# Performance work log

Measured on AMD Instinct MI355X. Metric: run time of the kernel, lower is better.

The kernel has to match this reference:

```python
import jax, jax.numpy as jnp
import numpy as np

B, L, H, M, V = 8, 1024, 1024, 128, 32
LN_EPS = 1e-5


def setup_inputs() -> dict:
    key = jax.random.key(0)
    ks = jax.random.split(key, 6)
    x_enc = jax.random.normal(ks[0], (B, L, H), dtype=jnp.float32)
    ln_gamma = jnp.ones((H,), jnp.float32)
    ln_beta = jnp.zeros((H,), jnp.float32)
    Wq = jax.random.normal(ks[1], (H, H), jnp.float32) * 0.02
    Wk = jax.random.normal(ks[2], (H, H), jnp.float32) * 0.02
    W_embed = jax.random.normal(ks[3], (V * V, H), jnp.float32) * 0.02
    W_mlm = jax.random.normal(ks[4], (V, H), jnp.float32) * 0.02
    # masked positions per sequence: contiguous span [1, M] (token 0 at pos 0,
    # token 2 at pos M+1 in the original encoding); sorted, in-range, static M.
    mask_idx = jnp.tile(jnp.arange(1, M + 1, dtype=jnp.int32)[None, :], (B, 1))
    return {"x_enc": x_enc, "ln_gamma": ln_gamma, "ln_beta": ln_beta,
            "Wq": Wq, "Wk": Wk, "W_embed": W_embed, "W_mlm": W_mlm,
            "mask_idx": mask_idx}


def _layer_norm(x, gamma, beta):
    mu = jnp.mean(x, axis=-1, keepdims=True)
    var = jnp.mean(jnp.square(x - mu), axis=-1, keepdims=True)
    return (x - mu) * jax.lax.rsqrt(var + LN_EPS) * gamma + beta


def reference(x_enc, ln_gamma, ln_beta, Wq, Wk, W_embed, W_mlm, mask_idx):
    x = _layer_norm(x_enc, ln_gamma, ln_beta)            # [B,L,H]
    mlm_logits = jnp.einsum('blh,vh->blv', x, W_mlm)      # [B,L,V]

    # ragged masked-span gather (static M masked positions per sequence)
    masked_x = jnp.take_along_axis(x, mask_idx[:, :, None].astype(jnp.int32), axis=1)  # [B,M,H]
    q = jnp.einsum('bmh,oh->bmo', masked_x, Wq)           # fc_pmlm_q, no bias
    k = jnp.einsum('bmh,oh->bmo', masked_x, Wk)           # fc_pmlm_k, no bias
    pairs = jnp.einsum('bih,bjh->bijh', q, k)             # per-span outer product [B,M,M,H]
    pairs = pairs.reshape(B * M * M, H)
    logits = jnp.einsum('nh,vh->nv', pairs, W_embed)      # [B*M*M, V*V]

    diag_mask = jnp.tile(jnp.eye(M, dtype=bool).reshape(-1), B)  # [B*M*M]

    in_span = jnp.zeros((B, L), jnp.int8).at[jnp.arange(B)[:, None], mask_idx].set(1)
    mask_aa = in_span[:, :, None]                                      # [B,L,1]
    pair_mask_aa = (in_span[:, :, None] * in_span[:, None, :])[..., None]  # [B,L,L,1] int8

    return logits, mlm_logits, diag_mask, mask_aa, pair_mask_aa
```

## Files before the change

kernel.cpp:

```cpp
#include <hip/hip_runtime.h>


typedef float   f32x4 __attribute__((ext_vector_type(4)));
typedef _Float16 f16x8 __attribute__((ext_vector_type(8)));

__device__ __forceinline__ void gld16(const void* g, void* l) {
  __builtin_amdgcn_global_load_lds(
      (const __attribute__((address_space(1))) void*)g,
      (__attribute__((address_space(3))) void*)l, 16, 0, 0);
}

__global__ __launch_bounds__(256) void cvt_kernel(
    const float* __restrict__ wq, const float* __restrict__ wk,
    const float* __restrict__ we, const float* __restrict__ wm,
    _Float16* __restrict__ oq, _Float16* __restrict__ ok,
    _Float16* __restrict__ oe, _Float16* __restrict__ om) {
  int id = blockIdx.x * 256 + threadIdx.x;
  const float* src; _Float16* dst; int off;
  if (id < 262144)      { src = wq; dst = oq; off = id; }
  else if (id < 524288) { src = wk; dst = ok; off = id - 262144; }
  else if (id < 786432) { src = we; dst = oe; off = id - 524288; }
  else                  { src = wm; dst = om; off = id - 786432; }
  float4 v = ((const float4*)src)[off];
  union { _Float16 h[4]; uint2 u; } o;
  o.h[0] = (_Float16)v.x; o.h[1] = (_Float16)v.y;
  o.h[2] = (_Float16)v.z; o.h[3] = (_Float16)v.w;
  ((uint2*)dst)[off] = o.u;
}

__global__ __launch_bounds__(256) void ln_kernel(
    const float* __restrict__ x, const float* __restrict__ g,
    const float* __restrict__ be, _Float16* __restrict__ xo) {
  const int row = blockIdx.x, t = threadIdx.x;
  const float4 v = ((const float4*)(x + (size_t)row * 1024))[t];
  float s1 = v.x + v.y + v.z + v.w;
  float s2 = v.x * v.x + v.y * v.y + v.z * v.z + v.w * v.w;
  #pragma unroll
  for (int m = 1; m < 64; m <<= 1) {
    s1 += __shfl_xor(s1, m, 64);
    s2 += __shfl_xor(s2, m, 64);
  }
  __shared__ float red[8];
  const int w = t >> 6, lane = t & 63;
  if (lane == 0) { red[w * 2] = s1; red[w * 2 + 1] = s2; }
  __syncthreads();
  s1 = red[0] + red[2] + red[4] + red[6];
  s2 = red[1] + red[3] + red[5] + red[7];
  const float mu = s1 * (1.f / 1024.f);
  const float var = s2 * (1.f / 1024.f) - mu * mu;
  const float rs = rsqrtf(var + 1e-5f);
  const float4 gv = ((const float4*)g)[t];
  const float4 bv = ((const float4*)be)[t];
  union { _Float16 h[4]; uint2 u; } o;
  o.h[0] = (_Float16)((v.x - mu) * rs * gv.x + bv.x);
  o.h[1] = (_Float16)((v.y - mu) * rs * gv.y + bv.y);
  o.h[2] = (_Float16)((v.z - mu) * rs * gv.z + bv.z);
  o.h[3] = (_Float16)((v.w - mu) * rs * gv.w + bv.w);
  ((uint2*)(xo + (size_t)row * 1024))[t] = o.u;
}

__global__ __launch_bounds__(256, 4) void qk_gemm(
    const _Float16* __restrict__ xh, const _Float16* __restrict__ wq,
    const _Float16* __restrict__ wk, const int* __restrict__ midx,
    _Float16* __restrict__ qout, _Float16* __restrict__ kout) {
  __shared__ _Float16 at[64 * 32];
  __shared__ _Float16 bt[64 * 32];
  const int tid = threadIdx.x, w = tid >> 6, lane = tid & 63;
  const int l15 = lane & 15, quad = lane >> 4;
  const int ntile = blockIdx.x, rtile = blockIdx.y, mat = blockIdx.z;
  const _Float16* wmat = mat ? wk : wq;
  _Float16* outp = mat ? kout : qout;

  const int arow = tid >> 2;
  const int acol = (tid & 3) * 8;
  const int grow = rtile * 64 + arow;
  const int b = grow >> 7, m = grow & 127;
  const int src = midx[b * 128 + m];
  const _Float16* agp = xh + ((size_t)(b * 1024 + src)) * 1024 + acol;
  const _Float16* bgp = wmat + (size_t)(ntile * 64 + arow) * 1024 + acol;
  char* aldst = (char*)at + w * 1024;
  char* bldst = (char*)bt + w * 1024;

  f32x4 acc[4];
  const f32x4 zero = {0.f, 0.f, 0.f, 0.f};
  #pragma unroll
  for (int ns = 0; ns < 4; ++ns) acc[ns] = zero;

  for (int s = 0; s < 32; ++s) {
    const int kk = s * 32;
    gld16(agp + kk, aldst);
    gld16(bgp + kk, bldst);
    __syncthreads();
    const f16x8 af = *(const f16x8*)&at[(w * 16 + l15) * 32 + quad * 8];
    #pragma unroll
    for (int ns = 0; ns < 4; ++ns) {
      const f16x8 bf = *(const f16x8*)&bt[(ns * 16 + l15) * 32 + quad * 8];
      acc[ns] = __builtin_amdgcn_mfma_f32_16x16x32_f16(af, bf, acc[ns], 0, 0, 0);
    }
    __syncthreads();
  }
  #pragma unroll
  for (int ns = 0; ns < 4; ++ns) {
    const int col = ntile * 64 + ns * 16 + l15;
    #pragma unroll
    for (int r = 0; r < 4; ++r) {
      const int row = rtile * 64 + w * 16 + quad * 4 + r;
      outp[(size_t)row * 1024 + col] = (_Float16)acc[ns][r];
    }
  }
}

#define BG_BUF 49152
#define BG_Q   147456
#define BG_WE  16384
__global__ __launch_bounds__(512, 2) void big_gemm(
    const _Float16* __restrict__ qf, const _Float16* __restrict__ kf,
    const _Float16* __restrict__ wemb, float* __restrict__ out) {
  __shared__ __align__(16) char lds[155648];
  const int tid = threadIdx.x;
  const int w = tid >> 6, lane = tid & 63;
  const int l15 = lane & 15, quad = lane >> 4;
  const int wm = w >> 2, wn = w & 3;
  const int bid = blockIdx.x;
  const int vtile = bid & 3;
  const int grp = bid >> 2;
  const int b = grp >> 3;
  const int i0base = (grp & 7) * 16;

  const int lrow = lane >> 3;
  const int cgsw = (lane & 7) ^ lrow;
  const char* kg = (const char*)(kf + (size_t)b * 128 * 1024);
  const char* wg = (const char*)(wemb + (size_t)vtile * 256 * 1024);
  const char* ks0 = kg + (size_t)(((w)      * 8 + lrow) * 2048 + cgsw * 16);
  const char* ks1 = kg + (size_t)(((w + 8)  * 8 + lrow) * 2048 + cgsw * 16);
  const char* ws0 = wg + (size_t)(((w)      * 8 + lrow) * 2048 + cgsw * 16);
  const char* ws1 = wg + (size_t)(((w + 8)  * 8 + lrow) * 2048 + cgsw * 16);
  const char* ws2 = wg + (size_t)(((w + 16) * 8 + lrow) * 2048 + cgsw * 16);
  const char* ws3 = wg + (size_t)(((w + 24) * 8 + lrow) * 2048 + cgsw * 16);
  const int kd0 = w * 1024,          kd1 = (w + 8) * 1024;
  const int wd0 = BG_WE + w * 1024,  wd1 = BG_WE + (w + 8) * 1024;
  const int wd2 = BG_WE + (w + 16) * 1024, wd3 = BG_WE + (w + 24) * 1024;

  const char* qsp = (const char*)(qf + (size_t)(b * 128 + i0base) * 1024)
                    + (w >> 1) * 2048 + (w & 1) * 1024 + lane * 16;

  const int swzb = (l15 & 7) << 4;
  const int col0 = (quad * 16) ^ swzb;
  const int col1 = (64 + quad * 16) ^ swzb;
  const int abase = l15 * 128;
  const int bbase = BG_WE + (wn * 64 + l15) * 128;
  const int qrd = BG_Q + wm * 2048 + quad * 16;

  if (w < 4) gld16(qsp, lds + BG_Q + w * 1024);
  gld16(ks0, lds + kd0);              gld16(ks1, lds + kd1);
  gld16(ws0, lds + wd0);              gld16(ws1, lds + wd1);
  gld16(ws2, lds + wd2);              gld16(ws3, lds + wd3);
  gld16(ks0 + 128, lds + BG_BUF + kd0); gld16(ks1 + 128, lds + BG_BUF + kd1);
  gld16(ws0 + 128, lds + BG_BUF + wd0); gld16(ws1 + 128, lds + BG_BUF + wd1);
  gld16(ws2 + 128, lds + BG_BUF + wd2); gld16(ws3 + 128, lds + BG_BUF + wd3);

  f32x4 acc[8][4];
  #pragma unroll
  for (int a = 0; a < 8; ++a)
    #pragma unroll
    for (int c = 0; c < 4; ++c) acc[a][c] = (f32x4){0.f, 0.f, 0.f, 0.f};

  f16x8 af[4][2], bf0[2][2], bf1[2][2], qs0, qs1;

#define RD_A(mh)                                                               \
  _Pragma("unroll")                                                            \
  for (int ms = 0; ms < 4; ++ms) {                                             \
    af[ms][0] = *(const f16x8*)(lds + cb + abase + (mh) * 8192 + ms * 2048 + col0); \
    af[ms][1] = *(const f16x8*)(lds + cb + abase + (mh) * 8192 + ms * 2048 + col1); \
  }
#define RD_B(dst, nh)                                                          \
  _Pragma("unroll")                                                            \
  for (int ns = 0; ns < 2; ++ns) {                                             \
    dst[ns][0] = *(const f16x8*)(lds + cb + bbase + (nh) * 4096 + ns * 2048 + col0); \
    dst[ns][1] = *(const f16x8*)(lds + cb + bbase + (nh) * 4096 + ns * 2048 + col1); \
  }
#define MULT_A()                                                               \
  _Pragma("unroll")                                                            \
  for (int ms = 0; ms < 4; ++ms) { af[ms][0] *= qs0; af[ms][1] *= qs1; }
#define MFMA8(MH, NH, BFR)                                                     \
  _Pragma("unroll")                                                            \
  for (int kh = 0; kh < 2; ++kh)                                               \
    _Pragma("unroll")                                                          \
    for (int ms = 0; ms < 4; ++ms)                                             \
      _Pragma("unroll")                                                        \
      for (int ns = 0; ns < 2; ++ns)                                           \
        acc[(MH) * 4 + ms][(NH) * 2 + ns] = __builtin_amdgcn_mfma_f32_16x16x32_f16( \
            af[ms][kh], BFR[ns][kh], acc[(MH) * 4 + ms][(NH) * 2 + ns], 0, 0, 0);
#define BAR() __builtin_amdgcn_s_barrier()
#define LGKM0() asm volatile("s_waitcnt lgkmcnt(0)" ::: "memory")

  int cur = 0;
  #pragma unroll 1
  for (int T = 0; T < 128; ++T) {
    const int cb = cur * BG_BUF;
    int stg = cur + 2; if (stg >= 3) stg -= 3;
    const int sb = stg * BG_BUF;
    const int j = T >> 4, tt = T & 15;
    const int skb = ((T + 2) & 15) * 128;
    const bool st = (T < 126);
    const bool stq = (w < 4) && (((T + 2) & 15) == 0) && (T + 2 < 128);

    if (T < 127) asm volatile("s_waitcnt vmcnt(6)" ::: "memory");
    else         asm volatile("s_waitcnt vmcnt(0)" ::: "memory");
    BAR();

    qs0 = *(const f16x8*)(lds + qrd + (j & 1) * 4096 + tt * 128);
    qs1 = *(const f16x8*)(lds + qrd + (j & 1) * 4096 + tt * 128 + 64);
    RD_A(0)
    RD_B(bf0, 0)
    if (stq) gld16(qsp + (T + 2) * 256,
                   lds + BG_Q + ((((T + 2) >> 4) & 1) * 4096) + w * 1024);
    if (st) { gld16(ks0 + skb, lds + sb + kd0); gld16(ks1 + skb, lds + sb + kd1); }
    BAR(); LGKM0();
    __builtin_amdgcn_s_setprio(1);
    MULT_A()
    MFMA8(0, 0, bf0)
    __builtin_amdgcn_s_setprio(0);
    BAR();
    RD_B(bf1, 1)
    if (st) { gld16(ws0 + skb, lds + sb + wd0); gld16(ws1 + skb, lds + sb + wd1); }
    BAR(); LGKM0();
    __builtin_amdgcn_s_setprio(1);
    MFMA8(0, 1, bf1)
    __builtin_amdgcn_s_setprio(0);
    BAR();
    RD_A(1)
    if (st) { gld16(ws2 + skb, lds + sb + wd2); gld16(ws3 + skb, lds + sb + wd3); }
    BAR(); LGKM0();
    __builtin_amdgcn_s_setprio(1);
    MULT_A()
    MFMA8(1, 1, bf1)
    MFMA8(1, 0, bf0)
    __builtin_amdgcn_s_setprio(0);
    BAR();

    cur = cur + 1; if (cur == 3) cur = 0;

    if (tt == 15) {
      const size_t nb = (size_t)(b * 128 + i0base + 2 * j + wm) * 128;
      const int colb = vtile * 256 + wn * 64;
      #pragma unroll
      for (int ms = 0; ms < 8; ++ms) {
        #pragma unroll
        for (int ns = 0; ns < 4; ++ns) {
          #pragma unroll
          for (int r = 0; r < 4; ++r)
            out[(nb + ms * 16 + quad * 4 + r) * 1024 + colb + ns * 16 + l15] =
                acc[ms][ns][r];
        }
      }
      #pragma unroll
      for (int a = 0; a < 8; ++a)
        #pragma unroll
        for (int c = 0; c < 4; ++c) acc[a][c] = (f32x4){0.f, 0.f, 0.f, 0.f};
    }
  }
#undef RD_A
#undef RD_B
#undef MULT_A
#undef MFMA8
#undef BAR
#undef LGKM0
}

__global__ __launch_bounds__(256) void mlm_kernel(
    const _Float16* __restrict__ xh, const _Float16* __restrict__ wm,
    float* __restrict__ out) {
  const int w = threadIdx.x >> 6, lane = threadIdx.x & 63;
  const int row = blockIdx.x * 4 + w;
  const int v = lane & 31, part = lane >> 5;
  const f16x8* xr = (const f16x8*)(xh + (size_t)row * 1024 + part * 512);
  const f16x8* wr = (const f16x8*)(wm + (size_t)v * 1024 + part * 512);
  float acc = 0.f;
  #pragma unroll 8
  for (int it = 0; it < 64; ++it) {
    const f16x8 p = xr[it] * wr[it];
    #pragma unroll
    for (int e = 0; e < 8; ++e) acc += (float)p[e];
  }
  acc += __shfl_xor(acc, 32, 64);
  if (part == 0) out[(size_t)row * 32 + v] = acc;
}

__global__ __launch_bounds__(256) void span_kernel(
    const int* __restrict__ midx, float* __restrict__ mask_aa,
    float* __restrict__ diag, float* __restrict__ span_ws) {
  __shared__ float flag[1024];
  const int b = blockIdx.x, t = threadIdx.x;
  for (int p = t; p < 1024; p += 256) flag[p] = 0.f;
  __syncthreads();
  if (t < 128) flag[midx[b * 128 + t]] = 1.f;
  __syncthreads();
  for (int p = t; p < 1024; p += 256) {
    const float f = flag[p];
    mask_aa[b * 1024 + p] = f;
    span_ws[b * 1024 + p] = f;
  }
  for (int p = t; p < 16384; p += 256)
    diag[b * 16384 + p] = ((p >> 7) == (p & 127)) ? 1.f : 0.f;
}

__global__ __launch_bounds__(256) void pairmask_kernel(
    const float* __restrict__ span_ws, float* __restrict__ out) {
  const int id = blockIdx.x * 256 + threadIdx.x;
  const int b = id >> 18;
  const int rem = id & 262143;
  const int i = rem >> 8;
  const int j4 = rem & 255;
  const float si = span_ws[b * 1024 + i];
  const float4 sj = ((const float4*)(span_ws + b * 1024))[j4];
  float4 o;
  o.x = si * sj.x; o.y = si * sj.y; o.z = si * sj.z; o.w = si * sj.w;
  ((float4*)out)[id] = o;
}

extern "C" void kernel_launch(void* const* d_in, const int* in_sizes, int n_in,
                              void* d_out, int out_size, void* d_ws, size_t ws_size,
                              hipStream_t stream) {
  const float* x_enc = (const float*)d_in[0];
  const float* gam   = (const float*)d_in[1];
  const float* bet   = (const float*)d_in[2];
  const float* Wq    = (const float*)d_in[3];
  const float* Wk    = (const float*)d_in[4];
  const float* We    = (const float*)d_in[5];
  const float* Wm    = (const float*)d_in[6];
  const int*   midx  = (const int*)d_in[7];
  float* out = (float*)d_out;

  char* ws = (char*)d_ws;
  _Float16* x_h  = (_Float16*)(ws);
  _Float16* q_h  = (_Float16*)(ws + ((size_t)16 << 20));
  _Float16* k_h  = (_Float16*)(ws + ((size_t)18 << 20));
  _Float16* wq_h = (_Float16*)(ws + ((size_t)20 << 20));
  _Float16* wk_h = (_Float16*)(ws + ((size_t)22 << 20));
  _Float16* we_h = (_Float16*)(ws + ((size_t)24 << 20));
  _Float16* wm_h = (_Float16*)(ws + ((size_t)26 << 20));
  float* span_ws = (float*)(ws + ((size_t)27 << 20));

  float* o_logits = out;
  float* o_mlm    = out + (size_t)134217728;
  float* o_diag   = o_mlm + 262144;
  float* o_maskaa = o_diag + 131072;
  float* o_pair   = o_maskaa + 8192;

  cvt_kernel<<<3104, 256, 0, stream>>>(Wq, Wk, We, Wm, wq_h, wk_h, we_h, wm_h);
  ln_kernel<<<8192, 256, 0, stream>>>(x_enc, gam, bet, x_h);
  qk_gemm<<<dim3(16, 16, 2), 256, 0, stream>>>(x_h, wq_h, wk_h, midx, q_h, k_h);
  big_gemm<<<dim3(256), 512, 0, stream>>>(q_h, k_h, we_h, o_logits);
  mlm_kernel<<<2048, 256, 0, stream>>>(x_h, wm_h, o_mlm);
  span_kernel<<<8, 256, 0, stream>>>(midx, o_maskaa, o_diag, span_ws);
  pairmask_kernel<<<8192, 256, 0, stream>>>(span_ws, o_pair);
}
```

Baseline: 874.6 us.

## Restructure big_gemm warp tiling, transpose epilogue via DPP for vector stores, defer epilogue

```diff
diff --git a/kernel.cpp b/kernel.cpp
--- a/kernel.cpp
+++ b/kernel.cpp
@@ -8,6 +8,15 @@
   __builtin_amdgcn_global_load_lds(
       (const __attribute__((address_space(1))) void*)g,
       (__attribute__((address_space(3))) void*)l, 16, 0, 0);
+}
+
+__device__ __forceinline__ float dpp_xor1(float x) {
+  return __builtin_bit_cast(float, __builtin_amdgcn_update_dpp(
+      0, __builtin_bit_cast(int, x), 177, 0xF, 0xF, false));
+}
+__device__ __forceinline__ float dpp_xor2(float x) {
+  return __builtin_bit_cast(float, __builtin_amdgcn_update_dpp(
+      0, __builtin_bit_cast(int, x), 78, 0xF, 0xF, false));
 }
 
 __global__ __launch_bounds__(256) void cvt_kernel(
@@ -111,8 +120,8 @@
 }
 
 #define BG_BUF 49152
+#define BG_WE  16384
 #define BG_Q   147456
-#define BG_WE  16384
 __global__ __launch_bounds__(512, 2) void big_gemm(
     const _Float16* __restrict__ qf, const _Float16* __restrict__ kf,
     const _Float16* __restrict__ wemb, float* __restrict__ out) {
@@ -120,7 +129,7 @@
   const int tid = threadIdx.x;
   const int w = tid >> 6, lane = tid & 63;
   const int l15 = lane & 15, quad = lane >> 4;
-  const int wm = w >> 2, wn = w & 3;
+  const int wj = w >> 2, wn = w & 3;
   const int bid = blockIdx.x;
   const int vtile = bid & 3;
   const int grp = bid >> 2;
@@ -147,9 +156,9 @@
   const int swzb = (l15 & 7) << 4;
   const int col0 = (quad * 16) ^ swzb;
   const int col1 = (64 + quad * 16) ^ swzb;
-  const int abase = l15 * 128;
-  const int bbase = BG_WE + (wn * 64 + l15) * 128;
-  const int qrd = BG_Q + wm * 2048 + quad * 16;
+  const int arow = (wj * 64 + l15) * 128;
+  const int brow = BG_WE + (wn * 64 + l15) * 128;
+  const int qrd  = BG_Q + quad * 16;
 
   if (w < 4) gld16(qsp, lds + BG_Q + w * 1024);
   gld16(ks0, lds + kd0);              gld16(ks1, lds + kd1);
@@ -159,40 +168,61 @@
   gld16(ws0 + 128, lds + BG_BUF + wd0); gld16(ws1 + 128, lds + BG_BUF + wd1);
   gld16(ws2 + 128, lds + BG_BUF + wd2); gld16(ws3 + 128, lds + BG_BUF + wd3);
 
-  f32x4 acc[8][4];
+  f32x4 acc[2][4][4];
   #pragma unroll
-  for (int a = 0; a < 8; ++a)
-    #pragma unroll
-    for (int c = 0; c < 4; ++c) acc[a][c] = (f32x4){0.f, 0.f, 0.f, 0.f};
-
-  f16x8 af[4][2], bf0[2][2], bf1[2][2], qs0, qs1;
-
-#define RD_A(mh)                                                               \
+  for (int ii = 0; ii < 2; ++ii)
+    #pragma unroll
+    for (int ms = 0; ms < 4; ++ms)
+      #pragma unroll
+      for (int vf = 0; vf < 4; ++vf) acc[ii][ms][vf] = (f32x4){0.f, 0.f, 0.f, 0.f};
+
+  f16x8 kfr[4][2], bf[4][2], qs[2][2], af[2];
+
+#define MM(AF, KH, II, MS)                                                     \
   _Pragma("unroll")                                                            \
-  for (int ms = 0; ms < 4; ++ms) {                                             \
-    af[ms][0] = *(const f16x8*)(lds + cb + abase + (mh) * 8192 + ms * 2048 + col0); \
-    af[ms][1] = *(const f16x8*)(lds + cb + abase + (mh) * 8192 + ms * 2048 + col1); \
-  }
-#define RD_B(dst, nh)                                                          \
+  for (int vf = 0; vf < 4; ++vf)                                               \
+    acc[II][MS][vf] = __builtin_amdgcn_mfma_f32_16x16x32_f16(                  \
+        AF, bf[vf][KH], acc[II][MS][vf], 0, 0, 0);
+
+#define GRP(II, KH)                                                            \
+  af[0] = kfr[0][KH] * qs[II][KH]; af[1] = kfr[1][KH] * qs[II][KH];            \
+  MM(af[0], KH, II, 0) MM(af[1], KH, II, 1)                                    \
+  af[0] = kfr[2][KH] * qs[II][KH]; af[1] = kfr[3][KH] * qs[II][KH];            \
+  MM(af[0], KH, II, 2) MM(af[1], KH, II, 3)
+
+#define BAR() __builtin_amdgcn_s_barrier()
+#define LGKM0() asm volatile("s_waitcnt lgkmcnt(0)" ::: "memory")
+
+#define EPILOGUE(JP) {                                                         \
+  const size_t nb0 = (size_t)(b * 128 + i0base + 2 * (JP)) * 128;              \
+  const int cb2 = vtile * 256 + wn * 64 + (l15 & 12);                          \
+  const int p = lane & 3;                                                      \
   _Pragma("unroll")                                                            \
-  for (int ns = 0; ns < 2; ++ns) {                                             \
-    dst[ns][0] = *(const f16x8*)(lds + cb + bbase + (nh) * 4096 + ns * 2048 + col0); \
-    dst[ns][1] = *(const f16x8*)(lds + cb + bbase + (nh) * 4096 + ns * 2048 + col1); \
-  }
-#define MULT_A()                                                               \
-  _Pragma("unroll")                                                            \
-  for (int ms = 0; ms < 4; ++ms) { af[ms][0] *= qs0; af[ms][1] *= qs1; }
-#define MFMA8(MH, NH, BFR)                                                     \
-  _Pragma("unroll")                                                            \
-  for (int kh = 0; kh < 2; ++kh)                                               \
+  for (int ii = 0; ii < 2; ++ii)                                               \
     _Pragma("unroll")                                                          \
     for (int ms = 0; ms < 4; ++ms)                                             \
       _Pragma("unroll")                                                        \
-      for (int ns = 0; ns < 2; ++ns)                                           \
-        acc[(MH) * 4 + ms][(NH) * 2 + ns] = __builtin_amdgcn_mfma_f32_16x16x32_f16( \
-            af[ms][kh], BFR[ns][kh], acc[(MH) * 4 + ms][(NH) * 2 + ns], 0, 0, 0);
-#define BAR() __builtin_amdgcn_s_barrier()
-#define LGKM0() asm volatile("s_waitcnt lgkmcnt(0)" ::: "memory")
+      for (int vf = 0; vf < 4; ++vf) {                                         \
+        f32x4 a = acc[ii][ms][vf];                                             \
+        float t0 = dpp_xor2(a[2]), t1 = dpp_xor2(a[3]);                        \
+        float t2 = dpp_xor2(a[0]), t3 = dpp_xor2(a[1]);                        \
+        float b0 = (p & 2) ? t0 : a[0];                                        \
+        float b1 = (p & 2) ? t1 : a[1];                                        \
+        float b2 = (p & 2) ? a[2] : t2;                                        \
+        float b3 = (p & 2) ? a[3] : t3;                                        \
+        float u0 = dpp_xor1(b1), u1 = dpp_xor1(b0);                            \
+        float u2 = dpp_xor1(b3), u3 = dpp_xor1(b2);                            \
+        f32x4 c;                                                               \
+        c[0] = (p & 1) ? u0 : b0;                                              \
+        c[1] = (p & 1) ? b1 : u1;                                              \
+        c[2] = (p & 1) ? u2 : b2;                                              \
+        c[3] = (p & 1) ? b3 : u3;                                              \
+        const size_t orow = nb0 + (size_t)ii * 128 + wj * 64 + ms * 16         \
+                            + quad * 4 + p;                                    \
+        *(f32x4*)(out + orow * 1024 + cb2 + vf * 16) = c;                      \
+        acc[ii][ms][vf] = (f32x4){0.f, 0.f, 0.f, 0.f};                         \
+      }                                                                        \
+}
 
   int cur = 0;
   #pragma unroll 1
@@ -200,72 +230,67 @@
     const int cb = cur * BG_BUF;
     int stg = cur + 2; if (stg >= 3) stg -= 3;
     const int sb = stg * BG_BUF;
-    const int j = T >> 4, tt = T & 15;
+    const int jit = T >> 4, tt = T & 15;
     const int skb = ((T + 2) & 15) * 128;
     const bool st = (T < 126);
     const bool stq = (w < 4) && (((T + 2) & 15) == 0) && (T + 2 < 128);
 
-    if (T < 127) asm volatile("s_waitcnt vmcnt(6)" ::: "memory");
-    else         asm volatile("s_waitcnt vmcnt(0)" ::: "memory");
-    BAR();
-
-    qs0 = *(const f16x8*)(lds + qrd + (j & 1) * 4096 + tt * 128);
-    qs1 = *(const f16x8*)(lds + qrd + (j & 1) * 4096 + tt * 128 + 64);
-    RD_A(0)
-    RD_B(bf0, 0)
+    if (T == 127)               asm volatile("s_waitcnt vmcnt(0)" ::: "memory");
+    else if (tt == 1 && T > 16) asm volatile("s_waitcnt vmcnt(38)" ::: "memory");
+    else                        asm volatile("s_waitcnt vmcnt(6)" ::: "memory");
+    BAR();
+
+    if (tt == 0 && T > 0) EPILOGUE(jit - 1)
+
+    qs[0][0] = *(const f16x8*)(lds + qrd + (jit & 1) * 4096 + tt * 128);
+    qs[1][0] = *(const f16x8*)(lds + qrd + (jit & 1) * 4096 + 2048 + tt * 128);
+    #pragma unroll
+    for (int ms = 0; ms < 4; ++ms)
+      kfr[ms][0] = *(const f16x8*)(lds + cb + arow + ms * 2048 + col0);
+    #pragma unroll
+    for (int vf = 0; vf < 4; ++vf)
+      bf[vf][0] = *(const f16x8*)(lds + cb + brow + vf * 2048 + col0);
     if (stq) gld16(qsp + (T + 2) * 256,
                    lds + BG_Q + ((((T + 2) >> 4) & 1) * 4096) + w * 1024);
     if (st) { gld16(ks0 + skb, lds + sb + kd0); gld16(ks1 + skb, lds + sb + kd1); }
     BAR(); LGKM0();
     __builtin_amdgcn_s_setprio(1);
-    MULT_A()
-    MFMA8(0, 0, bf0)
+    GRP(0, 0)
     __builtin_amdgcn_s_setprio(0);
     BAR();
-    RD_B(bf1, 1)
+
+    qs[0][1] = *(const f16x8*)(lds + qrd + (jit & 1) * 4096 + tt * 128 + 64);
+    qs[1][1] = *(const f16x8*)(lds + qrd + (jit & 1) * 4096 + 2048 + tt * 128 + 64);
+    #pragma unroll
+    for (int ms = 0; ms < 4; ++ms)
+      kfr[ms][1] = *(const f16x8*)(lds + cb + arow + ms * 2048 + col1);
+    #pragma unroll
+    for (int vf = 0; vf < 4; ++vf)
+      bf[vf][1] = *(const f16x8*)(lds + cb + brow + vf * 2048 + col1);
     if (st) { gld16(ws0 + skb, lds + sb + wd0); gld16(ws1 + skb, lds + sb + wd1); }
-    BAR(); LGKM0();
+    BAR();
     __builtin_amdgcn_s_setprio(1);
-    MFMA8(0, 1, bf1)
+    GRP(1, 0)
     __builtin_amdgcn_s_setprio(0);
     BAR();
-    RD_A(1)
+
     if (st) { gld16(ws2 + skb, lds + sb + wd2); gld16(ws3 + skb, lds + sb + wd3); }
     BAR(); LGKM0();
     __builtin_amdgcn_s_setprio(1);
-    MULT_A()
-    MFMA8(1, 1, bf1)
-    MFMA8(1, 0, bf0)
+    GRP(0, 1)
+    GRP(1, 1)
     __builtin_amdgcn_s_setprio(0);
     BAR();
 
     cur = cur + 1; if (cur == 3) cur = 0;
-
-    if (tt == 15) {
-      const size_t nb = (size_t)(b * 128 + i0base + 2 * j + wm) * 128;
-      const int colb = vtile * 256 + wn * 64;
-      #pragma unroll
-      for (int ms = 0; ms < 8; ++ms) {
-        #pragma unroll
-        for (int ns = 0; ns < 4; ++ns) {
-          #pragma unroll
-          for (int r = 0; r < 4; ++r)
-            out[(nb + ms * 16 + quad * 4 + r) * 1024 + colb + ns * 16 + l15] =
-                acc[ms][ns][r];
-        }
-      }
-      #pragma unroll
-      for (int a = 0; a < 8; ++a)
-        #pragma unroll
-        for (int c = 0; c < 4; ++c) acc[a][c] = (f32x4){0.f, 0.f, 0.f, 0.f};
-    }
-  }
-#undef RD_A
-#undef RD_B
-#undef MULT_A
-#undef MFMA8
+  }
+
+  EPILOGUE(7)
+#undef MM
+#undef GRP
 #undef BAR
 #undef LGKM0
+#undef EPILOGUE
 }
 
 __global__ __launch_bounds__(256) void mlm_kernel(
```

Measured after the change: 895.9 us. 1.02x slower.
